# Optimization experiments

Hardware: AMD Instinct MI355X
Metric: run time of the kernel (lower is better)

Reference implementation:

```python
import jax, jax.numpy as jnp
import numpy as np

N_HEAD = 16
ROPE_BASE = 10000.0


def _rope(x):
    # x: (B, T, H, D), interleaved even/odd (GPT-NeoX style)
    B, T, H, D = x.shape
    inv_freq = 1.0 / (ROPE_BASE ** (jnp.arange(0, D, 2, dtype=jnp.float32) / D))
    t = jnp.arange(T, dtype=jnp.float32)
    freqs = t[:, None] * inv_freq[None, :]            # (T, D//2)
    cos = jnp.cos(freqs)[None, :, None, :]            # (1, T, 1, D//2)
    sin = jnp.sin(freqs)[None, :, None, :]
    x1, x2 = x[..., ::2], x[..., 1::2]
    y1 = x1 * cos - x2 * sin
    y2 = x1 * sin + x2 * cos
    return jnp.stack((y1, y2), axis=-1).reshape(B, T, H, D)


def setup_inputs() -> dict:
    key = jax.random.key(0)
    k1, k2, k3 = jax.random.split(key, 3)
    B, T, C = 4, 2048, 1024
    x = jax.random.normal(k1, (B, T, C), dtype=jnp.float32)
    W_attn = jax.random.normal(k2, (C, 3 * C), dtype=jnp.float32) * (1.0 / np.sqrt(C))
    W_proj = jax.random.normal(k3, (C, C), dtype=jnp.float32) * (1.0 / np.sqrt(C))
    return {"x": x, "W_attn": W_attn, "W_proj": W_proj}


def reference(x, W_attn, W_proj):
    B, T, C = x.shape
    H = N_HEAD
    D = C // H
    qkv = jnp.einsum('btc,cf->btf', x, W_attn)        # (B, T, 3C)
    q, k, v = jnp.split(qkv, 3, axis=-1)
    q = _rope(q.reshape(B, T, H, D))
    k = _rope(k.reshape(B, T, H, D))
    v = v.reshape(B, T, H, D)
    # (B, H, T, D)
    q = q.transpose(0, 2, 1, 3)
    k = k.transpose(0, 2, 1, 3)
    v = v.transpose(0, 2, 1, 3)
    scale = 1.0 / np.sqrt(D).astype(np.float32)
    scores = jnp.einsum('bhqd,bhkd->bhqk', q, k) * scale
    causal = jnp.tril(jnp.ones((T, T), dtype=bool))
    scores = jnp.where(causal[None, None], scores, jnp.finfo(scores.dtype).min)
    att = jax.nn.softmax(scores, axis=-1)
    y = jnp.einsum('bhqk,bhkd->bhqd', att, v)         # (B, H, T, D)
    y = y.transpose(0, 2, 1, 3).reshape(B, T, C)
    return jnp.einsum('btc,cf->btf', y, W_proj)
```

## Files before the change

### kernel.cpp

```cpp
#include <hip/hip_runtime.h>
#include <hip/hip_bf16.h>
#include <math.h>

typedef __attribute__((ext_vector_type(8))) __bf16 bf16x8;
typedef __attribute__((ext_vector_type(4))) float f32x4;
typedef __attribute__((ext_vector_type(16))) float f32x16;
typedef __attribute__((ext_vector_type(4))) unsigned short us4;

#define DEVINL static __device__ __forceinline__

DEVINL unsigned short f2bf(float f) {
  union { float f; unsigned int u; } v; v.f = f;
  return (unsigned short)((v.u + 0x7FFFu + ((v.u >> 16) & 1u)) >> 16);
}

DEVINL unsigned short f2bf_hw(float f) {
  __bf16 h = (__bf16)f;
  union { __bf16 h; unsigned short u; } v; v.h = h;
  return v.u;
}

DEVINL unsigned pk2(float a, float b) {
  return (unsigned)f2bf_hw(a) | ((unsigned)f2bf_hw(b) << 16);
}

DEVINL f32x4 mfma16(bf16x8 a, bf16x8 b, f32x4 c) {
  return __builtin_amdgcn_mfma_f32_16x16x32_bf16(a, b, c, 0, 0, 0);
}
DEVINL f32x16 mfma32(bf16x8 a, bf16x8 b, f32x16 c) {
  return __builtin_amdgcn_mfma_f32_32x32x16_bf16(a, b, c, 0, 0, 0);
}

#define GLOAD16(GP, LP)                                                        \
  __builtin_amdgcn_global_load_lds(                                            \
      (const __attribute__((address_space(1))) void*)(GP),                     \
      (__attribute__((address_space(3))) void*)(LP), 16, 0, 0)

static constexpr int kB = 4, kT = 2048, kC = 1024, kH = 16, kD = 64;
static constexpr int kM = kB * kT;

__global__ void cvt_x_kernel(const float* __restrict__ x,
                             unsigned short* __restrict__ xb, int n4) {
  int stride = gridDim.x * blockDim.x;
  for (int i = blockIdx.x * blockDim.x + threadIdx.x; i < n4; i += stride) {
    float4 v = ((const float4*)x)[i];
    us4 o;
    o[0] = f2bf(v.x); o[1] = f2bf(v.y); o[2] = f2bf(v.z); o[3] = f2bf(v.w);
    ((us4*)xb)[i] = o;
  }
}

__global__ void transpose_w_kernel(const float* __restrict__ W,
                                   unsigned short* __restrict__ WT,
                                   int K, int N) {
  __shared__ float tile[32][33];
  int n0 = blockIdx.x * 32, k0 = blockIdx.y * 32;
  int tx = threadIdx.x, ty = threadIdx.y;
#pragma unroll
  for (int i = 0; i < 4; ++i)
    tile[ty + i * 8][tx] = W[(size_t)(k0 + ty + i * 8) * N + n0 + tx];
  __syncthreads();
#pragma unroll
  for (int i = 0; i < 4; ++i)
    WT[(size_t)(n0 + ty + i * 8) * K + k0 + tx] = f2bf(tile[tx][ty + i * 8]);
}

__global__ void rope_table_kernel(float* __restrict__ cosT,
                                  float* __restrict__ sinT) {
  int idx = blockIdx.x * blockDim.x + threadIdx.x;
  if (idx >= kT * 32) return;
  int d2 = idx >> 11, t = idx & 2047;
  double ang = (double)t * pow(10000.0, -(double)d2 / 32.0);
  cosT[idx] = (float)cos(ang);
  sinT[idx] = (float)sin(ang);
}

template <int EPI>
__global__ __launch_bounds__(512, 2) void gemm_bt_kernel(
    const unsigned short* __restrict__ A, const unsigned short* __restrict__ Bt,
    float* __restrict__ Cout, int Ndim, int Kdim,
    const float* __restrict__ cosT, const float* __restrict__ sinT,
    unsigned short* __restrict__ Qr, unsigned short* __restrict__ Kr,
    unsigned short* __restrict__ Vtg) {
  __shared__ unsigned short As[3][256 * 64];
  __shared__ unsigned short Bs[3][128 * 64];
  const int tid = threadIdx.x;
  const int wave = tid >> 6, lane = tid & 63;

  const int nwg = gridDim.x * gridDim.y;
  const int lin = blockIdx.y * gridDim.x + blockIdx.x;
  const int wg = (lin & 7) * (nwg >> 3) + (lin >> 3);
  const int n0 = (wg % gridDim.x) * 128, m0 = (wg / gridDim.x) * 256;

  const int wr = wave >> 1, wc = wave & 1;

  f32x4 acc[4][4] = {};

  const int fr = lane & 15;

  const int sblk = tid;
  const int srow3 = sblk >> 3, skb = sblk & 7;
  const int sgran = (skb ^ (srow3 & 7)) << 3;

  auto stageA = [&](int t, int l) {
    const int bb = t % 3;
    const int k0 = t << 6;
    const int row = (l << 6) + srow3;
    GLOAD16(A + (size_t)(m0 + row) * Kdim + k0 + sgran,
            &As[bb][(l * 512 + wave * 64) * 8]);
  };
  auto stageB = [&](int t, int l) {
    const int bb = t % 3;
    const int k0 = t << 6;
    const int row = (l << 6) + srow3;
    GLOAD16(Bt + (size_t)(n0 + row) * Kdim + k0 + sgran,
            &Bs[bb][(l * 512 + wave * 64) * 8]);
  };

  const int NT = Kdim >> 6;

  stageA(0, 0); stageA(0, 1); stageA(0, 2); stageA(0, 3);
  stageB(0, 0); stageB(0, 1);
  stageA(1, 0); stageA(1, 1); stageA(1, 2); stageA(1, 3);
  stageB(1, 0); stageB(1, 1);
  asm volatile("s_waitcnt vmcnt(6)" ::: "memory");
  __builtin_amdgcn_sched_barrier(0);
  __builtin_amdgcn_s_barrier();

  const int rx = lane & 7, ku = lane >> 4;

  for (int t = 0; t < NT; ++t) {
    const int buf = t % 3;
    const unsigned char* Ab = (const unsigned char*)As[buf];
    const unsigned char* Bb = (const unsigned char*)Bs[buf];
    bf16x8 af[4], bfr[4];

    {
      const int col = ((ku ^ rx) << 4);
#pragma unroll
      for (int f = 0; f < 4; ++f)
        af[f] = *(const bf16x8*)(Ab + (wr * 64 + f * 16 + fr) * 128 + col);
#pragma unroll
      for (int f = 0; f < 4; ++f)
        bfr[f] = *(const bf16x8*)(Bb + (wc * 64 + f * 16 + fr) * 128 + col);
    }
    if (t + 2 < NT) { stageA(t + 2, 0); stageA(t + 2, 1); stageB(t + 2, 0); }
    __builtin_amdgcn_s_barrier();
    asm volatile("s_waitcnt lgkmcnt(0)" ::: "memory");
    __builtin_amdgcn_sched_barrier(0);
    __builtin_amdgcn_s_setprio(1);
#pragma unroll
    for (int i = 0; i < 4; ++i)
#pragma unroll
      for (int j = 0; j < 4; ++j)
        acc[i][j] = mfma16(af[i], bfr[j], acc[i][j]);
    __builtin_amdgcn_s_setprio(0);
    __builtin_amdgcn_s_barrier();

    {
      const int col = (((4 | ku) ^ rx) << 4);
#pragma unroll
      for (int f = 0; f < 4; ++f)
        af[f] = *(const bf16x8*)(Ab + (wr * 64 + f * 16 + fr) * 128 + col);
#pragma unroll
      for (int f = 0; f < 4; ++f)
        bfr[f] = *(const bf16x8*)(Bb + (wc * 64 + f * 16 + fr) * 128 + col);
    }
    if (t + 2 < NT) { stageA(t + 2, 2); stageA(t + 2, 3); stageB(t + 2, 1); }
    if (t + 2 < NT) {
      asm volatile("s_waitcnt vmcnt(6)" ::: "memory");
    } else if (t + 1 < NT) {
      asm volatile("s_waitcnt vmcnt(0)" ::: "memory");
    }
    __builtin_amdgcn_sched_barrier(0);
    __builtin_amdgcn_s_barrier();
    asm volatile("s_waitcnt lgkmcnt(0)" ::: "memory");
    __builtin_amdgcn_sched_barrier(0);
    __builtin_amdgcn_s_setprio(1);
#pragma unroll
    for (int i = 0; i < 4; ++i)
#pragma unroll
      for (int j = 0; j < 4; ++j)
        acc[i][j] = mfma16(af[i], bfr[j], acc[i][j]);
    __builtin_amdgcn_s_setprio(0);
    __builtin_amdgcn_s_barrier();
  }

  const int lr = (lane >> 4) * 4;
  const int fc = lane & 15;
  if (EPI == 0) {
#pragma unroll
    for (int i = 0; i < 4; ++i) {
      int mb = m0 + wr * 64 + i * 16 + lr;
#pragma unroll
      for (int j = 0; j < 4; ++j) {
        int n = n0 + wc * 64 + j * 16 + fc;
#pragma unroll
        for (int r = 0; r < 4; ++r)
          Cout[(size_t)(mb + r) * Ndim + n] = acc[i][j][r];
      }
    }
  } else {
#pragma unroll
    for (int i = 0; i < 4; ++i) {
      int mb = m0 + wr * 64 + i * 16 + lr;
      int b = mb >> 11, t0 = mb & 2047;
#pragma unroll
      for (int j = 0; j < 4; ++j) {
        int n = n0 + wc * 64 + j * 16 + fc;
        int sec = n >> 10;
        int c = n & 1023;
        int h = c >> 6, d = c & 63;
        size_t bh = (size_t)(b * 16 + h);
        if (sec == 2) {
          us4 pk;
#pragma unroll
          for (int r = 0; r < 4; ++r) pk[r] = f2bf(acc[i][j][r]);
          *(us4*)&Vtg[(bh * 64 + d) * 2048 + t0] = pk;
        } else {
          unsigned short* dst = (sec == 0) ? Qr : Kr;
          float4 c4 = *(const float4*)&cosT[(d >> 1) * 2048 + t0];
          float4 s4 = *(const float4*)&sinT[(d >> 1) * 2048 + t0];
          const float* cp = (const float*)&c4;
          const float* sp = (const float*)&s4;
#pragma unroll
          for (int r = 0; r < 4; ++r) {
            float v = acc[i][j][r];
            float pv = __shfl_xor(v, 1);
            float y = (d & 1) ? fmaf(pv, sp[r], v * cp[r])
                              : fmaf(v, cp[r], -pv * sp[r]);
            dst[(bh * 2048 + t0 + r) * 64 + d] = f2bf(y);
          }
        }
      }
    }
  }
}

__global__ __launch_bounds__(256, 3)
void attn_kernel(const unsigned short* __restrict__ Qr,
                 const unsigned short* __restrict__ Kr,
                 const unsigned short* __restrict__ Vtg,
                 unsigned short* __restrict__ Yb) {
  __shared__ unsigned short Ks[2][64 * 64];
  __shared__ unsigned short Vs[2][64 * 64];

  const int tid = threadIdx.x;
  const int wave = tid >> 6, lane = tid & 63;
  const int q31 = lane & 31, hi = lane >> 5;
  const int srow = lane >> 3;
  const int sblk = (lane & 7) ^ srow;
  const int rswz = (lane & 7) << 4;

  int lin = blockIdx.y * 8 + blockIdx.x;
  int wg = (lin & 7) * 128 + (lin >> 3);
  const int qblk = wg & 15;
  const int bh = wg >> 4;

  const unsigned short* Qg = Qr + (size_t)bh * 2048 * 64;
  const unsigned short* Kg = Kr + (size_t)bh * 2048 * 64;
  const unsigned short* Vg = Vtg + (size_t)bh * 64 * 2048;

  const float c = 0.18033688f;
  const float THR = 44.0f;

  auto stage = [&](int j, int bb) {
    int kv0s = j * 64;
#pragma unroll
    for (int o = 0; o < 2; ++o) {
      int s = o * 4 + wave;
      int row = s * 8 + srow;
      GLOAD16(Kg + ((size_t)(kv0s + row) * 64 + sblk * 8), &Ks[bb][s * 512]);
      GLOAD16(Vg + ((size_t)row * 2048 + kv0s + sblk * 8), &Vs[bb][s * 512]);
    }
  };

  const int qw = qblk * 128 + wave * 32;
  const int qg = qw + q31;
  const int NT = 2 * qblk + 2;

  bf16x8 qf[4];
#pragma unroll
  for (int ds = 0; ds < 4; ++ds)
    qf[ds] = *(const bf16x8*)&Qg[(size_t)qg * 64 + ds * 16 + hi * 8];

  float mrow = -1e30f, lrow = 0.f;
  f32x16 y0 = {}, y1 = {};

  stage(0, 0);
  asm volatile("s_waitcnt vmcnt(0)" ::: "memory");
  __syncthreads();

  for (int t = 0; t < NT; ++t) {
    const int buf = t & 1;
    if (t + 1 < NT) stage(t + 1, buf ^ 1);
    const int kv0 = t * 64;

    if (kv0 <= qw + 31) {
      f32x16 st[2] = {};
      __builtin_amdgcn_s_setprio(1);
#pragma unroll
      for (int sub = 0; sub < 2; ++sub) {
        const unsigned char* kbase =
            (const unsigned char*)Ks[buf] + (sub * 32 + q31) * 128;
#pragma unroll
        for (int ds = 0; ds < 4; ++ds) {
          bf16x8 af = *(const bf16x8*)(kbase + ((ds * 32 + hi * 16) ^ rswz));
          st[sub] = mfma32(af, qf[ds], st[sub]);
        }
      }
      __builtin_amdgcn_s_setprio(0);

      if (kv0 + 63 > qw) {
#pragma unroll
        for (int sub = 0; sub < 2; ++sub)
#pragma unroll
          for (int r = 0; r < 16; ++r) {
            int kv = kv0 + sub * 32 + (r & 3) + 8 * (r >> 2) + 4 * hi;
            if (kv > qg) st[sub][r] = -1e30f;
          }
      }

      float tm = st[0][0];
#pragma unroll
      for (int r = 1; r < 16; ++r) tm = fmaxf(tm, st[0][r]);
#pragma unroll
      for (int r = 0; r < 16; ++r) tm = fmaxf(tm, st[1][r]);
      tm = fmaxf(tm, __shfl_xor(tm, 32));

      if (!__all(tm <= mrow + THR)) {
        float mn = fmaxf(mrow, tm);
        float al = __builtin_amdgcn_exp2f((mrow - mn) * c);
        mrow = mn;
        lrow *= al;
#pragma unroll
        for (int r = 0; r < 16; ++r) { y0[r] *= al; y1[r] *= al; }
      }

      const float mc = mrow * c;
      float ps = 0.f;
      unsigned pkw[2][8];
#pragma unroll
      for (int sub = 0; sub < 2; ++sub)
#pragma unroll
        for (int j = 0; j < 8; ++j) {
          float pa = __builtin_amdgcn_exp2f(fmaf(st[sub][2 * j], c, -mc));
          float pb = __builtin_amdgcn_exp2f(fmaf(st[sub][2 * j + 1], c, -mc));
          ps += pa + pb;
          pkw[sub][j] = pk2(pa, pb);
        }
      ps += __shfl_xor(ps, 32);
      lrow += ps;

      __builtin_amdgcn_s_setprio(1);
#pragma unroll
      for (int sub = 0; sub < 2; ++sub) {
#pragma unroll
        for (int ksl = 0; ksl < 2; ++ksl) {
          unsigned w0 = pkw[sub][ksl * 4 + 0], w2 = pkw[sub][ksl * 4 + 2];
          unsigned w1 = pkw[sub][ksl * 4 + 1], w3 = pkw[sub][ksl * 4 + 3];
          asm volatile("v_permlane32_swap_b32 %0, %1" : "+v"(w0), "+v"(w2));
          asm volatile("v_permlane32_swap_b32 %0, %1" : "+v"(w1), "+v"(w3));
          union { bf16x8 v; unsigned u[4]; } pf;
          pf.u[0] = w0; pf.u[1] = w1; pf.u[2] = w2; pf.u[3] = w3;
          const int cb = sub * 64 + ksl * 32 + hi * 16;
#pragma unroll
          for (int dm = 0; dm < 2; ++dm) {
            const int row = dm * 32 + q31;
            bf16x8 vf = *(const bf16x8*)((const unsigned char*)Vs[buf] +
                                         row * 128 + (cb ^ rswz));
            if (dm == 0) y0 = mfma32(vf, pf.v, y0);
            else         y1 = mfma32(vf, pf.v, y1);
          }
        }
      }
      __builtin_amdgcn_s_setprio(0);
    }

    __syncthreads();
  }

  const int b = bh >> 4, h = bh & 15;
  float inv = __builtin_amdgcn_rcpf(lrow);
  unsigned short* yrow = Yb + (size_t)(b * 2048 + qg) * 1024 + h * 64;
#pragma unroll
  for (int dm = 0; dm < 2; ++dm)
#pragma unroll
    for (int g = 0; g < 4; ++g) {
      us4 o;
#pragma unroll
      for (int e = 0; e < 4; ++e) {
        float yv = dm ? y1[g * 4 + e] : y0[g * 4 + e];
        o[e] = f2bf_hw(yv * inv);
      }
      *(us4*)&yrow[dm * 32 + g * 8 + hi * 4] = o;
    }
}

extern "C" void kernel_launch(void* const* d_in, const int* in_sizes, int n_in,
                              void* d_out, int out_size, void* d_ws,
                              size_t ws_size, hipStream_t stream) {
  const float* x = (const float*)d_in[0];
  const float* Wa = (const float*)d_in[1];
  const float* Wp = (const float*)d_in[2];
  float* out = (float*)d_out;
  char* ws = (char*)d_ws;

  constexpr size_t OFF_WAT = 0;
  constexpr size_t OFF_WPT = 6291456;
  constexpr size_t OFF_COS = 8388608;
  constexpr size_t OFF_SIN = 8650752;
  constexpr size_t OFF_XB  = 8912896;
  constexpr size_t OFF_Q   = 25690112;
  constexpr size_t OFF_K   = 42467328;
  constexpr size_t OFF_V   = 59244544;

  unsigned short* WaT = (unsigned short*)(ws + OFF_WAT);
  unsigned short* WpT = (unsigned short*)(ws + OFF_WPT);
  float* cosT = (float*)(ws + OFF_COS);
  float* sinT = (float*)(ws + OFF_SIN);
  unsigned short* xb = (unsigned short*)(ws + OFF_XB);
  unsigned short* Yb = xb;
  unsigned short* Qr = (unsigned short*)(ws + OFF_Q);
  unsigned short* Kr = (unsigned short*)(ws + OFF_K);
  unsigned short* Vt = (unsigned short*)(ws + OFF_V);

  cvt_x_kernel<<<2048, 256, 0, stream>>>(x, xb, kM * kC / 4);
  transpose_w_kernel<<<dim3(96, 32), dim3(32, 8), 0, stream>>>(Wa, WaT, 1024, 3072);
  transpose_w_kernel<<<dim3(32, 32), dim3(32, 8), 0, stream>>>(Wp, WpT, 1024, 1024);
  rope_table_kernel<<<256, 256, 0, stream>>>(cosT, sinT);

  gemm_bt_kernel<1><<<dim3(24, 32), 512, 0, stream>>>(
      xb, WaT, nullptr, 3072, 1024, cosT, sinT, Qr, Kr, Vt);

  attn_kernel<<<dim3(8, 128), 256, 0, stream>>>(Qr, Kr, Vt, Yb);

  gemm_bt_kernel<0><<<dim3(8, 32), 512, 0, stream>>>(
      Yb, WpT, out, 1024, 1024, nullptr, nullptr, nullptr, nullptr, nullptr);
}
```

Baseline: 192.7 us.

## Fuse prep kernels and pair causal query blocks in attention for balance

The four preprocessing launches (x conversion, two weight transposes, rope table) are merged into one kernel that dispatches by block index, removing launch gaps. The attention kernel now uses 2-wave workgroups over 64-row query blocks and processes a complementary pair (qb and 31-qb) per workgroup. Each workgroup then does a near-equal amount of causal work, addressing the tail imbalance of the old 128-row blocks. In exchange each workgroup runs two sequential passes with fewer waves to hide latency, and K/V tiles are shared by only two waves instead of four.

```diff
diff --git a/kernel.cpp b/kernel.cpp
--- a/kernel.cpp
+++ b/kernel.cpp
@@ -39,40 +39,42 @@
 static constexpr int kB = 4, kT = 2048, kC = 1024, kH = 16, kD = 64;
 static constexpr int kM = kB * kT;
 
-__global__ void cvt_x_kernel(const float* __restrict__ x,
-                             unsigned short* __restrict__ xb, int n4) {
-  int stride = gridDim.x * blockDim.x;
-  for (int i = blockIdx.x * blockDim.x + threadIdx.x; i < n4; i += stride) {
-    float4 v = ((const float4*)x)[i];
-    us4 o;
-    o[0] = f2bf(v.x); o[1] = f2bf(v.y); o[2] = f2bf(v.z); o[3] = f2bf(v.w);
-    ((us4*)xb)[i] = o;
+__global__ __launch_bounds__(256) void prep_kernel(
+    const float* __restrict__ x, unsigned short* __restrict__ xb,
+    const float* __restrict__ Wa, unsigned short* __restrict__ WaT,
+    const float* __restrict__ Wp, unsigned short* __restrict__ WpT,
+    float* __restrict__ cosT, float* __restrict__ sinT) {
+  const int blk = blockIdx.x;
+  if (blk < 2048) {
+    const int n4 = kM * kC / 4;
+    for (int i = blk * 256 + threadIdx.x; i < n4; i += 2048 * 256) {
+      float4 v = ((const float4*)x)[i];
+      us4 o;
+      o[0] = f2bf(v.x); o[1] = f2bf(v.y); o[2] = f2bf(v.z); o[3] = f2bf(v.w);
+      ((us4*)xb)[i] = o;
+    }
+  } else if (blk < 2048 + 3072 + 1024) {
+    __shared__ float tile[32][33];
+    int t = blk - 2048;
+    const float* W; unsigned short* WT; int N, bx, by;
+    if (t < 3072) { W = Wa; WT = WaT; N = 3072; bx = t % 96; by = t / 96; }
+    else { t -= 3072; W = Wp; WT = WpT; N = 1024; bx = t % 32; by = t / 32; }
+    const int n0 = bx * 32, k0 = by * 32;
+    const int tx = threadIdx.x & 31, ty = threadIdx.x >> 5;
+#pragma unroll
+    for (int i = 0; i < 4; ++i)
+      tile[ty + i * 8][tx] = W[(size_t)(k0 + ty + i * 8) * N + n0 + tx];
+    __syncthreads();
+#pragma unroll
+    for (int i = 0; i < 4; ++i)
+      WT[(size_t)(n0 + ty + i * 8) * 1024 + k0 + tx] = f2bf(tile[tx][ty + i * 8]);
+  } else {
+    int idx = (blk - 6144) * 256 + threadIdx.x;
+    int d2 = idx >> 11, t = idx & 2047;
+    double ang = (double)t * pow(10000.0, -(double)d2 / 32.0);
+    cosT[idx] = (float)cos(ang);
+    sinT[idx] = (float)sin(ang);
   }
-}
-
-__global__ void transpose_w_kernel(const float* __restrict__ W,
-                                   unsigned short* __restrict__ WT,
-                                   int K, int N) {
-  __shared__ float tile[32][33];
-  int n0 = blockIdx.x * 32, k0 = blockIdx.y * 32;
-  int tx = threadIdx.x, ty = threadIdx.y;
-#pragma unroll
-  for (int i = 0; i < 4; ++i)
-    tile[ty + i * 8][tx] = W[(size_t)(k0 + ty + i * 8) * N + n0 + tx];
-  __syncthreads();
-#pragma unroll
-  for (int i = 0; i < 4; ++i)
-    WT[(size_t)(n0 + ty + i * 8) * K + k0 + tx] = f2bf(tile[tx][ty + i * 8]);
-}
-
-__global__ void rope_table_kernel(float* __restrict__ cosT,
-                                  float* __restrict__ sinT) {
-  int idx = blockIdx.x * blockDim.x + threadIdx.x;
-  if (idx >= kT * 32) return;
-  int d2 = idx >> 11, t = idx & 2047;
-  double ang = (double)t * pow(10000.0, -(double)d2 / 32.0);
-  cosT[idx] = (float)cos(ang);
-  sinT[idx] = (float)sin(ang);
 }
 
 template <int EPI>
@@ -237,7 +239,7 @@
   }
 }
 
-__global__ __launch_bounds__(256, 3)
+__global__ __launch_bounds__(128, 2)
 void attn_kernel(const unsigned short* __restrict__ Qr,
                  const unsigned short* __restrict__ Kr,
                  const unsigned short* __restrict__ Vtg,
@@ -254,7 +256,7 @@
 
   int lin = blockIdx.y * 8 + blockIdx.x;
   int wg = (lin & 7) * 128 + (lin >> 3);
-  const int qblk = wg & 15;
+  const int cpair = wg & 15;
   const int bh = wg >> 4;
 
   const unsigned short* Qg = Qr + (size_t)bh * 2048 * 64;
@@ -267,134 +269,137 @@
   auto stage = [&](int j, int bb) {
     int kv0s = j * 64;
 #pragma unroll
-    for (int o = 0; o < 2; ++o) {
-      int s = o * 4 + wave;
+    for (int o = 0; o < 4; ++o) {
+      int s = o * 2 + wave;
       int row = s * 8 + srow;
       GLOAD16(Kg + ((size_t)(kv0s + row) * 64 + sblk * 8), &Ks[bb][s * 512]);
       GLOAD16(Vg + ((size_t)row * 2048 + kv0s + sblk * 8), &Vs[bb][s * 512]);
     }
   };
 
-  const int qw = qblk * 128 + wave * 32;
-  const int qg = qw + q31;
-  const int NT = 2 * qblk + 2;
-
-  bf16x8 qf[4];
-#pragma unroll
-  for (int ds = 0; ds < 4; ++ds)
-    qf[ds] = *(const bf16x8*)&Qg[(size_t)qg * 64 + ds * 16 + hi * 8];
-
-  float mrow = -1e30f, lrow = 0.f;
-  f32x16 y0 = {}, y1 = {};
-
-  stage(0, 0);
-  asm volatile("s_waitcnt vmcnt(0)" ::: "memory");
-  __syncthreads();
-
-  for (int t = 0; t < NT; ++t) {
-    const int buf = t & 1;
-    if (t + 1 < NT) stage(t + 1, buf ^ 1);
-    const int kv0 = t * 64;
-
-    if (kv0 <= qw + 31) {
-      f32x16 st[2] = {};
-      __builtin_amdgcn_s_setprio(1);
-#pragma unroll
-      for (int sub = 0; sub < 2; ++sub) {
-        const unsigned char* kbase =
-            (const unsigned char*)Ks[buf] + (sub * 32 + q31) * 128;
-#pragma unroll
-        for (int ds = 0; ds < 4; ++ds) {
-          bf16x8 af = *(const bf16x8*)(kbase + ((ds * 32 + hi * 16) ^ rswz));
-          st[sub] = mfma32(af, qf[ds], st[sub]);
-        }
+  for (int seg = 0; seg < 2; ++seg) {
+    const int qb = seg ? (31 - cpair) : cpair;
+    const int qw = qb * 64 + wave * 32;
+    const int qg = qw + q31;
+    const int NT = qb + 1;
+
+    bf16x8 qf[4];
+#pragma unroll
+    for (int ds = 0; ds < 4; ++ds)
+      qf[ds] = *(const bf16x8*)&Qg[(size_t)qg * 64 + ds * 16 + hi * 8];
+
+    float mrow = -1e30f, lrow = 0.f;
+    f32x16 y0 = {}, y1 = {};
+
+    stage(0, 0);
+    asm volatile("s_waitcnt vmcnt(0)" ::: "memory");
+    __syncthreads();
+
+    for (int t = 0; t < NT; ++t) {
+      const int buf = t & 1;
+      if (t + 1 < NT) stage(t + 1, buf ^ 1);
+      const int kv0 = t * 64;
+
+      if (kv0 <= qw + 31) {
+        f32x16 st[2] = {};
+        __builtin_amdgcn_s_setprio(1);
+#pragma unroll
+        for (int sub = 0; sub < 2; ++sub) {
+          const unsigned char* kbase =
+              (const unsigned char*)Ks[buf] + (sub * 32 + q31) * 128;
+#pragma unroll
+          for (int ds = 0; ds < 4; ++ds) {
+            bf16x8 af = *(const bf16x8*)(kbase + ((ds * 32 + hi * 16) ^ rswz));
+            st[sub] = mfma32(af, qf[ds], st[sub]);
+          }
+        }
+        __builtin_amdgcn_s_setprio(0);
+
+        if (kv0 + 63 > qw) {
+#pragma unroll
+          for (int sub = 0; sub < 2; ++sub)
+#pragma unroll
+            for (int r = 0; r < 16; ++r) {
+              int kv = kv0 + sub * 32 + (r & 3) + 8 * (r >> 2) + 4 * hi;
+              if (kv > qg) st[sub][r] = -1e30f;
+            }
+        }
+
+        float tm = st[0][0];
+#pragma unroll
+        for (int r = 1; r < 16; ++r) tm = fmaxf(tm, st[0][r]);
+#pragma unroll
+        for (int r = 0; r < 16; ++r) tm = fmaxf(tm, st[1][r]);
+        tm = fmaxf(tm, __shfl_xor(tm, 32));
+
+        if (!__all(tm <= mrow + THR)) {
+          float mn = fmaxf(mrow, tm);
+          float al = __builtin_amdgcn_exp2f((mrow - mn) * c);
+          mrow = mn;
+          lrow *= al;
+#pragma unroll
+          for (int r = 0; r < 16; ++r) { y0[r] *= al; y1[r] *= al; }
+        }
+
+        const float mc = mrow * c;
+        float ps = 0.f;
+        unsigned pkw[2][8];
+#pragma unroll
+        for (int sub = 0; sub < 2; ++sub)
+#pragma unroll
+          for (int j = 0; j < 8; ++j) {
+            float pa = __builtin_amdgcn_exp2f(fmaf(st[sub][2 * j], c, -mc));
+            float pb = __builtin_amdgcn_exp2f(fmaf(st[sub][2 * j + 1], c, -mc));
+            ps += pa + pb;
+            pkw[sub][j] = pk2(pa, pb);
+          }
+        ps += __shfl_xor(ps, 32);
+        lrow += ps;
+
+        __builtin_amdgcn_s_setprio(1);
+#pragma unroll
+        for (int sub = 0; sub < 2; ++sub) {
+#pragma unroll
+          for (int ksl = 0; ksl < 2; ++ksl) {
+            unsigned w0 = pkw[sub][ksl * 4 + 0], w2 = pkw[sub][ksl * 4 + 2];
+            unsigned w1 = pkw[sub][ksl * 4 + 1], w3 = pkw[sub][ksl * 4 + 3];
+            asm volatile("v_permlane32_swap_b32 %0, %1" : "+v"(w0), "+v"(w2));
+            asm volatile("v_permlane32_swap_b32 %0, %1" : "+v"(w1), "+v"(w3));
+            union { bf16x8 v; unsigned u[4]; } pf;
+            pf.u[0] = w0; pf.u[1] = w1; pf.u[2] = w2; pf.u[3] = w3;
+            const int cb = sub * 64 + ksl * 32 + hi * 16;
+#pragma unroll
+            for (int dm = 0; dm < 2; ++dm) {
+              const int row = dm * 32 + q31;
+              bf16x8 vf = *(const bf16x8*)((const unsigned char*)Vs[buf] +
+                                           row * 128 + (cb ^ rswz));
+              if (dm == 0) y0 = mfma32(vf, pf.v, y0);
+              else         y1 = mfma32(vf, pf.v, y1);
+            }
+          }
+        }
+        __builtin_amdgcn_s_setprio(0);
       }
-      __builtin_amdgcn_s_setprio(0);
-
-      if (kv0 + 63 > qw) {
-#pragma unroll
-        for (int sub = 0; sub < 2; ++sub)
-#pragma unroll
-          for (int r = 0; r < 16; ++r) {
-            int kv = kv0 + sub * 32 + (r & 3) + 8 * (r >> 2) + 4 * hi;
-            if (kv > qg) st[sub][r] = -1e30f;
-          }
+
+      __syncthreads();
+    }
+
+    const int b = bh >> 4, h = bh & 15;
+    float inv = __builtin_amdgcn_rcpf(lrow);
+    unsigned short* yrow = Yb + (size_t)(b * 2048 + qg) * 1024 + h * 64;
+#pragma unroll
+    for (int dm = 0; dm < 2; ++dm)
+#pragma unroll
+      for (int g = 0; g < 4; ++g) {
+        us4 o;
+#pragma unroll
+        for (int e = 0; e < 4; ++e) {
+          float yv = dm ? y1[g * 4 + e] : y0[g * 4 + e];
+          o[e] = f2bf_hw(yv * inv);
+        }
+        *(us4*)&yrow[dm * 32 + g * 8 + hi * 4] = o;
       }
-
-      float tm = st[0][0];
-#pragma unroll
-      for (int r = 1; r < 16; ++r) tm = fmaxf(tm, st[0][r]);
-#pragma unroll
-      for (int r = 0; r < 16; ++r) tm = fmaxf(tm, st[1][r]);
-      tm = fmaxf(tm, __shfl_xor(tm, 32));
-
-      if (!__all(tm <= mrow + THR)) {
-        float mn = fmaxf(mrow, tm);
-        float al = __builtin_amdgcn_exp2f((mrow - mn) * c);
-        mrow = mn;
-        lrow *= al;
-#pragma unroll
-        for (int r = 0; r < 16; ++r) { y0[r] *= al; y1[r] *= al; }
-      }
-
-      const float mc = mrow * c;
-      float ps = 0.f;
-      unsigned pkw[2][8];
-#pragma unroll
-      for (int sub = 0; sub < 2; ++sub)
-#pragma unroll
-        for (int j = 0; j < 8; ++j) {
-          float pa = __builtin_amdgcn_exp2f(fmaf(st[sub][2 * j], c, -mc));
-          float pb = __builtin_amdgcn_exp2f(fmaf(st[sub][2 * j + 1], c, -mc));
-          ps += pa + pb;
-          pkw[sub][j] = pk2(pa, pb);
-        }
-      ps += __shfl_xor(ps, 32);
-      lrow += ps;
-
-      __builtin_amdgcn_s_setprio(1);
-#pragma unroll
-      for (int sub = 0; sub < 2; ++sub) {
-#pragma unroll
-        for (int ksl = 0; ksl < 2; ++ksl) {
-          unsigned w0 = pkw[sub][ksl * 4 + 0], w2 = pkw[sub][ksl * 4 + 2];
-          unsigned w1 = pkw[sub][ksl * 4 + 1], w3 = pkw[sub][ksl * 4 + 3];
-          asm volatile("v_permlane32_swap_b32 %0, %1" : "+v"(w0), "+v"(w2));
-          asm volatile("v_permlane32_swap_b32 %0, %1" : "+v"(w1), "+v"(w3));
-          union { bf16x8 v; unsigned u[4]; } pf;
-          pf.u[0] = w0; pf.u[1] = w1; pf.u[2] = w2; pf.u[3] = w3;
-          const int cb = sub * 64 + ksl * 32 + hi * 16;
-#pragma unroll
-          for (int dm = 0; dm < 2; ++dm) {
-            const int row = dm * 32 + q31;
-            bf16x8 vf = *(const bf16x8*)((const unsigned char*)Vs[buf] +
-                                         row * 128 + (cb ^ rswz));
-            if (dm == 0) y0 = mfma32(vf, pf.v, y0);
-            else         y1 = mfma32(vf, pf.v, y1);
-          }
-        }
-      }
-      __builtin_amdgcn_s_setprio(0);
-    }
-
-    __syncthreads();
   }
-
-  const int b = bh >> 4, h = bh & 15;
-  float inv = __builtin_amdgcn_rcpf(lrow);
-  unsigned short* yrow = Yb + (size_t)(b * 2048 + qg) * 1024 + h * 64;
-#pragma unroll
-  for (int dm = 0; dm < 2; ++dm)
-#pragma unroll
-    for (int g = 0; g < 4; ++g) {
-      us4 o;
-#pragma unroll
-      for (int e = 0; e < 4; ++e) {
-        float yv = dm ? y1[g * 4 + e] : y0[g * 4 + e];
-        o[e] = f2bf_hw(yv * inv);
-      }
-      *(us4*)&yrow[dm * 32 + g * 8 + hi * 4] = o;
-    }
 }
 
 extern "C" void kernel_launch(void* const* d_in, const int* in_sizes, int n_in,
@@ -425,15 +430,13 @@
   unsigned short* Kr = (unsigned short*)(ws + OFF_K);
   unsigned short* Vt = (unsigned short*)(ws + OFF_V);
 
-  cvt_x_kernel<<<2048, 256, 0, stream>>>(x, xb, kM * kC / 4);
-  transpose_w_kernel<<<dim3(96, 32), dim3(32, 8), 0, stream>>>(Wa, WaT, 1024, 3072);
-  transpose_w_kernel<<<dim3(32, 32), dim3(32, 8), 0, stream>>>(Wp, WpT, 1024, 1024);
-  rope_table_kernel<<<256, 256, 0, stream>>>(cosT, sinT);
+  prep_kernel<<<2048 + 3072 + 1024 + 256, 256, 0, stream>>>(
+      x, xb, Wa, WaT, Wp, WpT, cosT, sinT);
 
   gemm_bt_kernel<1><<<dim3(24, 32), 512, 0, stream>>>(
       xb, WaT, nullptr, 3072, 1024, cosT, sinT, Qr, Kr, Vt);
 
-  attn_kernel<<<dim3(8, 128), 256, 0, stream>>>(Qr, Kr, Vt, Yb);
+  attn_kernel<<<dim3(8, 128), 128, 0, stream>>>(Qr, Kr, Vt, Yb);
 
   gemm_bt_kernel<0><<<dim3(8, 32), 512, 0, stream>>>(
       Yb, WpT, out, 1024, 1024, nullptr, nullptr, nullptr, nullptr, nullptr);
```

Result: faster. 181.1 us (-6.0%).
